# Kernel tuning notes

Measured on AMD Instinct MI355X. Metric: run time of the kernel, lower is better.

Reference implementation:

```python
import jax, jax.numpy as jnp
import numpy as np

B, T, I = 64, 512, 128
H, R, DA, C = 256, 20, 50, 10

def setup_inputs() -> dict:
    key = jax.random.key(0)
    ks = jax.random.split(key, 8)
    s = 0.05
    return {
        "x": jax.random.normal(ks[0], (B, T, I), dtype=jnp.float32),
        "W_ih": jax.random.normal(ks[1], (I, 4 * H), dtype=jnp.float32) * s,
        "W_hh": jax.random.normal(ks[2], (H, 4 * H), dtype=jnp.float32) * s,
        "b": jnp.zeros((4 * H,), dtype=jnp.float32),
        "W1": jax.random.normal(ks[3], (DA, I), dtype=jnp.float32) * s,
        "b1": jnp.zeros((DA,), dtype=jnp.float32),
        "W2": jax.random.normal(ks[4], (R, DA), dtype=jnp.float32) * s,
        "b2": jnp.zeros((R,), dtype=jnp.float32),
        "Wfc": jax.random.normal(ks[5], (C, H), dtype=jnp.float32) * s,
        "bfc": jnp.zeros((C,), dtype=jnp.float32),
    }

def reference(x, W_ih, W_hh, b, W1, b1, W2, b2, Wfc, bfc):
    # Dropout is identity (eval mode). Attention scores for all timesteps at once.
    bsz, seq, inp = x.shape
    hid = W_hh.shape[0]
    r = W2.shape[0]
    # scores: [B, T, r]
    S = jnp.tanh(jnp.einsum('bti,di->btd', x, W1) + b1)
    S = jnp.einsum('btd,rd->btr', S, W2) + b2
    # Prefix softmax over time via cumulative sums (softmax shift-invariant,
    # use global max over time per (b, r) for stability).
    E = jnp.exp(S - jnp.max(S, axis=1, keepdims=True))          # [B, T, r]
    denom = jnp.cumsum(E, axis=1)                               # [B, T, r]
    numer = jnp.cumsum(E[:, :, :, None] * x[:, :, None, :], axis=1)  # [B, T, r, I]
    M = jnp.mean(numer / denom[:, :, :, None], axis=2)          # [B, T, I]
    # Precompute input contribution to gates for all steps.
    gx = jnp.einsum('bti,ig->btg', M, W_ih) + b                 # [B, T, 4H]
    h0 = jnp.ones((bsz, hid), dtype=x.dtype)
    c0 = jnp.ones((bsz, hid), dtype=x.dtype)

    def step(carry, g_x):
        h, c = carry
        g = g_x + h @ W_hh
        i_t = jax.nn.sigmoid(g[:, :hid])
        f_t = jax.nn.sigmoid(g[:, hid:2 * hid])
        g_t = jnp.tanh(g[:, 2 * hid:3 * hid])
        o_t = jax.nn.sigmoid(g[:, 3 * hid:])
        c = f_t * c + i_t * g_t
        h = o_t * jnp.tanh(c)
        return (h, c), None

    (h_T, _), _ = jax.lax.scan(step, (h0, c0), jnp.swapaxes(gx, 0, 1))
    logits = h_T @ Wfc.T + bfc                                  # [B, C]
    return jax.nn.softmax(logits, axis=1)
```

## Files before the change

### kernel.cpp

```cpp
#include <hip/hip_runtime.h>
#include <hip/hip_fp16.h>

#define B_   64
#define T_   512
#define I_   128
#define H_   256
#define G4_  1024
#define R_   20
#define DA_  50
#define C_   10

typedef _Float16 half2_t __attribute__((ext_vector_type(2)));
typedef _Float16 half8_t __attribute__((ext_vector_type(8)));

union H8 {
  half8_t v8;
  half2_t h2[4];
};

__device__ __forceinline__ float fsigmoid(float x) {
  return __fdividef(1.0f, 1.0f + __expf(-x));
}
__device__ __forceinline__ float ftanh(float x) {
  return 1.0f - __fdividef(2.0f, __expf(2.0f * x) + 1.0f);
}

__global__ __launch_bounds__(256) void k0_pack(const float* __restrict__ Whh,
                                               half2_t* __restrict__ Wq) {
  int idx = blockIdx.x * 256 + threadIdx.x;
  int g = idx & 1023, k2 = idx >> 10;
  half2_t h;
  h.x = (_Float16)Whh[(2 * k2) * G4_ + g];
  h.y = (_Float16)Whh[(2 * k2 + 1) * G4_ + g];
  Wq[g * 128 + k2] = h;
}

__global__ __launch_bounds__(256) void k_init(unsigned long long* __restrict__ Hx) {
  int i = blockIdx.x * 256 + threadIdx.x;
  Hx[i] = 0ull;
}

__global__ __launch_bounds__(64) void k1_scores(const float* __restrict__ x,
                                                const float* __restrict__ W1,
                                                const float* __restrict__ b1,
                                                const float* __restrict__ W2,
                                                const float* __restrict__ b2,
                                                float* __restrict__ S) {
  int bt = blockIdx.x;
  int b = bt >> 9, t = bt & 511;
  int l = threadIdx.x;
  __shared__ float xs[I_];
  __shared__ float as[DA_];
  const float* xr = x + (size_t)bt * I_;
  xs[l] = xr[l];
  xs[l + 64] = xr[l + 64];
  __syncthreads();
  if (l < DA_) {
    float acc = b1[l];
    const float* wr = W1 + l * I_;
#pragma unroll 8
    for (int k = 0; k < I_; k++) acc += xs[k] * wr[k];
    as[l] = tanhf(acc);
  }
  __syncthreads();
  if (l < R_) {
    float acc = b2[l];
    const float* wr = W2 + l * DA_;
#pragma unroll 5
    for (int d = 0; d < DA_; d++) acc += as[d] * wr[d];
    S[((size_t)(b * R_ + l)) * T_ + t] = acc;
  }
}

__global__ __launch_bounds__(64) void k2_prefix(const float* __restrict__ S,
                                                float* __restrict__ E,
                                                float* __restrict__ invd) {
  int br = blockIdx.x;
  int l = threadIdx.x;
  const float* Sr = S + (size_t)br * T_;
  float v[8];
  float m = -1e30f;
#pragma unroll
  for (int c = 0; c < 8; c++) {
    v[c] = Sr[c * 64 + l];
    m = fmaxf(m, v[c]);
  }
#pragma unroll
  for (int off = 32; off; off >>= 1) m = fmaxf(m, __shfl_xor(m, off));
  float carry = 0.f;
  for (int c = 0; c < 8; c++) {
    float e = expf(v[c] - m);
    float s = e;
#pragma unroll
    for (int off = 1; off < 64; off <<= 1) {
      float u = __shfl_up(s, off);
      if (l >= off) s += u;
    }
    E[(size_t)br * T_ + c * 64 + l] = e;
    invd[(size_t)br * T_ + c * 64 + l] = 1.f / (carry + s);
    carry += __shfl(s, 63);
  }
}

__global__ __launch_bounds__(128) void k3_context(const float* __restrict__ x,
                                                  const float* __restrict__ E,
                                                  const float* __restrict__ invd,
                                                  float* __restrict__ M) {
  int b = blockIdx.x;
  int i = threadIdx.x;
  __shared__ float es[2][R_], ds[2][R_];
  float acc[R_];
#pragma unroll
  for (int r = 0; r < R_; r++) acc[r] = 0.f;
  float rE = 0.f, rD = 0.f;
  if (i < R_)
    rE = E[((size_t)(b * R_ + i)) * T_ + 0];
  else if (i < 2 * R_)
    rD = invd[((size_t)(b * R_ + (i - R_))) * T_ + 0];
  const float* xb = x + (size_t)b * T_ * I_;
  float xv = xb[i];
  int buf = 0;
  for (int t = 0; t < T_; t++) {
    if (i < R_) es[buf][i] = rE;
    else if (i < 2 * R_) ds[buf][i - R_] = rD;
    __syncthreads();
    if (t + 1 < T_) {
      if (i < R_)
        rE = E[((size_t)(b * R_ + i)) * T_ + t + 1];
      else if (i < 2 * R_)
        rD = invd[((size_t)(b * R_ + (i - R_))) * T_ + t + 1];
    }
    float xcur = xv;
    if (t + 1 < T_) xv = xb[(size_t)(t + 1) * I_ + i];
    float s = 0.f;
#pragma unroll
    for (int r = 0; r < R_; r++) {
      acc[r] += es[buf][r] * xcur;
      s += acc[r] * ds[buf][r];
    }
    M[(size_t)b * T_ * I_ + (size_t)t * I_ + i] = s * (1.0f / R_);
    buf ^= 1;
  }
}

__global__ __launch_bounds__(256) void k4_gemm(const float* __restrict__ Mm,
                                               const float* __restrict__ Wih,
                                               const float* __restrict__ bg,
                                               __half* __restrict__ gx) {
  __shared__ float As[I_][64];
  __shared__ float Bs[I_][64];
  int row0 = blockIdx.x * 64, col0 = blockIdx.y * 64;
  int tid = threadIdx.x;
#pragma unroll
  for (int ch = 0; ch < 8; ch++) {
    int fidx = ch * 256 + tid;
    int r = fidx >> 5;
    int kk = (fidx & 31) << 2;
    float4 f = ((const float4*)(Mm + (size_t)(row0 + r) * I_))[fidx & 31];
    As[kk + 0][r] = f.x;
    As[kk + 1][r] = f.y;
    As[kk + 2][r] = f.z;
    As[kk + 3][r] = f.w;
  }
#pragma unroll
  for (int ch = 0; ch < 8; ch++) {
    int fidx = ch * 256 + tid;
    int k = fidx >> 4;
    int c4 = (fidx & 15) << 2;
    float4 f = *((const float4*)(Wih + (size_t)k * G4_ + col0 + c4));
    *((float4*)&Bs[k][c4]) = f;
  }
  __syncthreads();
  int ty = tid >> 4, tx = tid & 15;
  float acc[4][4] = {};
#pragma unroll 4
  for (int k = 0; k < I_; k++) {
    float4 a = *((float4*)&As[k][ty << 2]);
    float4 bq = *((float4*)&Bs[k][tx << 2]);
    acc[0][0] += a.x * bq.x; acc[0][1] += a.x * bq.y; acc[0][2] += a.x * bq.z; acc[0][3] += a.x * bq.w;
    acc[1][0] += a.y * bq.x; acc[1][1] += a.y * bq.y; acc[1][2] += a.y * bq.z; acc[1][3] += a.y * bq.w;
    acc[2][0] += a.z * bq.x; acc[2][1] += a.z * bq.y; acc[2][2] += a.z * bq.z; acc[2][3] += a.z * bq.w;
    acc[3][0] += a.w * bq.x; acc[3][1] += a.w * bq.y; acc[3][2] += a.w * bq.z; acc[3][3] += a.w * bq.w;
  }
#pragma unroll
  for (int ii = 0; ii < 4; ii++) {
#pragma unroll
    for (int jj = 0; jj < 4; jj++) {
      int row = row0 + (ty << 2) + ii;
      int col = col0 + (tx << 2) + jj;
      gx[(size_t)row * G4_ + col] = __float2half(acc[ii][jj] + bg[col]);
    }
  }
}

__global__ __launch_bounds__(512, 2) void k5_lstm(
    const __half* __restrict__ gx, const half2_t* __restrict__ Wq,
    unsigned long long* __restrict__ Hx, float* __restrict__ hT) {
  int b = blockIdx.x & 63;
  int p = blockIdx.x >> 6;
  int tid = threadIdx.x;
  int kh = tid & 1;
  int c = tid >> 1;
  int gate = c >> 6, uloc = c & 63;
  int gcol = gate * 256 + p * 64 + uloc;

  __shared__ __align__(16) half2_t hs[H_ / 2];
  __shared__ float gsum[256];

  int qi = tid >> 5;
  int q = qi + (qi >= p ? 1 : 0);
  int d = tid & 31;

  H8 w[16];
  {
    const H8* wp = (const H8*)(Wq + (size_t)gcol * 128 + kh * 64);
#pragma unroll
    for (int i = 0; i < 16; i++) w[i].v8 = wp[i].v8;
  }
  asm volatile("" ::: "memory");

  float cstate = 1.0f;
  const __half* gxb = gx + (size_t)b * T_ * G4_;

  for (int t = 0; t < T_; t++) {
    float gxv = 0.f;
    if (!kh) gxv = (float)gxb[(size_t)t * G4_ + gcol];

    if (t == 0) {
      if (tid < 128) {
        half2_t o;
        o.x = (_Float16)1.0f;
        o.y = (_Float16)1.0f;
        hs[tid] = o;
      }
    } else if (tid < 96) {
      const unsigned long long* src =
          Hx + ((size_t)(t & 1) * 64 + b) * 128 + q * 32 + d;
      unsigned long long v;
      do {
        v = __hip_atomic_load(src, __ATOMIC_RELAXED, __HIP_MEMORY_SCOPE_AGENT);
      } while ((unsigned)(v >> 32) != (unsigned)t);
      ((unsigned*)hs)[q * 32 + d] = (unsigned)v;
    }
    __syncthreads();

    float a0 = 0.f, a1 = 0.f, a2 = 0.f, a3 = 0.f;
#pragma unroll
    for (int i = 0; i < 16; i++) {
      H8 hv;
      hv.v8 = *(const half8_t*)(hs + kh * 64 + i * 4);
      a0 = __builtin_amdgcn_fdot2(w[i].h2[0], hv.h2[0], a0, false);
      a1 = __builtin_amdgcn_fdot2(w[i].h2[1], hv.h2[1], a1, false);
      a2 = __builtin_amdgcn_fdot2(w[i].h2[2], hv.h2[2], a2, false);
      a3 = __builtin_amdgcn_fdot2(w[i].h2[3], hv.h2[3], a3, false);
    }
    float s = (a0 + a1) + (a2 + a3);
    s += __shfl_xor(s, 1);
    if (!kh) gsum[c] = s + gxv;
    __syncthreads();

    if (tid < 64) {
      float vi = gsum[tid], vf = gsum[64 + tid], vg = gsum[128 + tid],
            vo = gsum[192 + tid];
      vi = fsigmoid(vi);
      vf = fsigmoid(vf);
      vo = fsigmoid(vo);
      vg = ftanh(vg);
      cstate = vf * cstate + vi * vg;
      float h = vo * ftanh(cstate);
      unsigned hu = (unsigned)__half_as_ushort(__float2half(h));
      ((unsigned short*)hs)[p * 64 + tid] = (unsigned short)hu;
      unsigned hup = (unsigned)__shfl_xor((int)hu, 1);
      if (!(tid & 1) && (t + 1 < T_)) {
        unsigned long long pkt =
            (unsigned long long)(hu | (hup << 16)) |
            ((unsigned long long)(unsigned)(t + 1) << 32);
        unsigned long long* dst =
            Hx + ((size_t)((t + 1) & 1) * 64 + b) * 128 + p * 32 + (tid >> 1);
        __hip_atomic_store(dst, pkt, __ATOMIC_RELAXED,
                           __HIP_MEMORY_SCOPE_AGENT);
      }
      if (t == T_ - 1) hT[b * H_ + p * 64 + tid] = h;
    }
  }
}

__global__ __launch_bounds__(64) void k6_head(const float* __restrict__ hT,
                                              const float* __restrict__ Wfc,
                                              const float* __restrict__ bfc,
                                              float* __restrict__ out) {
  int b = blockIdx.x, l = threadIdx.x;
  const float* h = hT + b * H_;
  float p[C_];
#pragma unroll
  for (int c = 0; c < C_; c++) p[c] = 0.f;
#pragma unroll
  for (int q = 0; q < 4; q++) {
    float hv = h[q * 64 + l];
#pragma unroll
    for (int c = 0; c < C_; c++) p[c] += hv * Wfc[c * H_ + q * 64 + l];
  }
#pragma unroll
  for (int c = 0; c < C_; c++)
    for (int off = 32; off; off >>= 1) p[c] += __shfl_xor(p[c], off);
  if (l == 0) {
    float m = -1e30f, e[C_], sum = 0.f;
    for (int c = 0; c < C_; c++) { p[c] += bfc[c]; m = fmaxf(m, p[c]); }
    for (int c = 0; c < C_; c++) { e[c] = expf(p[c] - m); sum += e[c]; }
    for (int c = 0; c < C_; c++) out[b * C_ + c] = e[c] / sum;
  }
}

extern "C" void kernel_launch(void* const* d_in, const int* in_sizes, int n_in,
                              void* d_out, int out_size, void* d_ws, size_t ws_size,
                              hipStream_t stream) {
  const float* x   = (const float*)d_in[0];
  const float* Wih = (const float*)d_in[1];
  const float* Whh = (const float*)d_in[2];
  const float* bg  = (const float*)d_in[3];
  const float* W1  = (const float*)d_in[4];
  const float* b1  = (const float*)d_in[5];
  const float* W2  = (const float*)d_in[6];
  const float* b2  = (const float*)d_in[7];
  const float* Wfc = (const float*)d_in[8];
  const float* bfc = (const float*)d_in[9];
  float* out = (float*)d_out;

  float* wsf = (float*)d_ws;
  unsigned long long* Hx = (unsigned long long*)wsf;
  float* S    = wsf;
  float* E    = wsf + 655360;
  float* INVD = wsf + 1310720;
  float* Mm   = wsf + 1966080;
  float* hT   = wsf + 6160384;
  half2_t* Wq = (half2_t*)(wsf + 6176768);
  __half* gx  = (__half*)(wsf + 6307840);

  hipLaunchKernelGGL(k0_pack,   dim3(512),      dim3(256), 0, stream, Whh, Wq);
  hipLaunchKernelGGL(k1_scores, dim3(B_ * T_),  dim3(64),  0, stream, x, W1, b1, W2, b2, S);
  hipLaunchKernelGGL(k2_prefix, dim3(B_ * R_),  dim3(64),  0, stream, S, E, INVD);
  hipLaunchKernelGGL(k3_context,dim3(B_),       dim3(128), 0, stream, x, E, INVD, Mm);
  hipLaunchKernelGGL(k4_gemm,   dim3(512, 16),  dim3(256), 0, stream, Mm, Wih, bg, gx);
  hipLaunchKernelGGL(k_init,    dim3(64),       dim3(256), 0, stream, Hx);
  hipLaunchKernelGGL(k5_lstm,   dim3(256),      dim3(512), 0, stream, gx, Wq, Hx, hT);
  hipLaunchKernelGGL(k6_head,   dim3(B_),       dim3(64),  0, stream, hT, Wfc, bfc, out);
}
```

Measured before the change: 1.407 ms.

## Tile score GEMM, chunk context scan over time, and shuffle-based LSTM gate combine

```diff
diff --git a/kernel.cpp b/kernel.cpp
--- a/kernel.cpp
+++ b/kernel.cpp
@@ -13,11 +13,6 @@
 typedef _Float16 half2_t __attribute__((ext_vector_type(2)));
 typedef _Float16 half8_t __attribute__((ext_vector_type(8)));
 
-union H8 {
-  half8_t v8;
-  half2_t h2[4];
-};
-
 __device__ __forceinline__ float fsigmoid(float x) {
   return __fdividef(1.0f, 1.0f + __expf(-x));
 }
@@ -40,35 +35,68 @@
   Hx[i] = 0ull;
 }
 
-__global__ __launch_bounds__(64) void k1_scores(const float* __restrict__ x,
-                                                const float* __restrict__ W1,
-                                                const float* __restrict__ b1,
-                                                const float* __restrict__ W2,
-                                                const float* __restrict__ b2,
-                                                float* __restrict__ S) {
-  int bt = blockIdx.x;
+__global__ __launch_bounds__(256) void k1_scores(const float* __restrict__ x,
+                                                 const float* __restrict__ W1,
+                                                 const float* __restrict__ b1,
+                                                 const float* __restrict__ W2,
+                                                 const float* __restrict__ b2,
+                                                 float* __restrict__ S) {
+  __shared__ float xs[64][129];
+  __shared__ float w1s[128][64];
+  __shared__ float a1s[64][53];
+  int blk = blockIdx.x;
+  int tid = threadIdx.x;
+  int row0 = blk * 64;
+  const float4* xv = (const float4*)(x + (size_t)row0 * I_);
+#pragma unroll
+  for (int ch = 0; ch < 8; ch++) {
+    int fidx = ch * 256 + tid;
+    int r = fidx >> 5, k4 = (fidx & 31) << 2;
+    float4 f = xv[fidx];
+    xs[r][k4] = f.x; xs[r][k4 + 1] = f.y; xs[r][k4 + 2] = f.z; xs[r][k4 + 3] = f.w;
+  }
+  const float4* w1v = (const float4*)W1;
+#pragma unroll
+  for (int ch = 0; ch < 7; ch++) {
+    int fidx = ch * 256 + tid;
+    if (fidx < 1600) {
+      int d = fidx >> 5, k4 = (fidx & 31) << 2;
+      float4 f = w1v[fidx];
+      w1s[k4][d] = f.x; w1s[k4 + 1][d] = f.y; w1s[k4 + 2][d] = f.z; w1s[k4 + 3][d] = f.w;
+    }
+  }
+  __syncthreads();
+  int ty = tid >> 4, tx = tid & 15;
+  float acc[4][4] = {};
+#pragma unroll 4
+  for (int k = 0; k < I_; k++) {
+    float a0 = xs[4 * ty][k], a1 = xs[4 * ty + 1][k];
+    float a2 = xs[4 * ty + 2][k], a3 = xs[4 * ty + 3][k];
+    float4 bq = *(const float4*)&w1s[k][tx << 2];
+    acc[0][0] += a0 * bq.x; acc[0][1] += a0 * bq.y; acc[0][2] += a0 * bq.z; acc[0][3] += a0 * bq.w;
+    acc[1][0] += a1 * bq.x; acc[1][1] += a1 * bq.y; acc[1][2] += a1 * bq.z; acc[1][3] += a1 * bq.w;
+    acc[2][0] += a2 * bq.x; acc[2][1] += a2 * bq.y; acc[2][2] += a2 * bq.z; acc[2][3] += a2 * bq.w;
+    acc[3][0] += a3 * bq.x; acc[3][1] += a3 * bq.y; acc[3][2] += a3 * bq.z; acc[3][3] += a3 * bq.w;
+  }
+#pragma unroll
+  for (int i = 0; i < 4; i++) {
+#pragma unroll
+    for (int j = 0; j < 4; j++) {
+      int col = (tx << 2) + j;
+      if (col < DA_) a1s[4 * ty + i][col] = tanhf(acc[i][j] + b1[col]);
+    }
+  }
+  __syncthreads();
+  int row = tid & 63, rq = tid >> 6;
+  int bt = row0 + row;
   int b = bt >> 9, t = bt & 511;
-  int l = threadIdx.x;
-  __shared__ float xs[I_];
-  __shared__ float as[DA_];
-  const float* xr = x + (size_t)bt * I_;
-  xs[l] = xr[l];
-  xs[l + 64] = xr[l + 64];
-  __syncthreads();
-  if (l < DA_) {
-    float acc = b1[l];
-    const float* wr = W1 + l * I_;
-#pragma unroll 8
-    for (int k = 0; k < I_; k++) acc += xs[k] * wr[k];
-    as[l] = tanhf(acc);
-  }
-  __syncthreads();
-  if (l < R_) {
-    float acc = b2[l];
-    const float* wr = W2 + l * DA_;
-#pragma unroll 5
-    for (int d = 0; d < DA_; d++) acc += as[d] * wr[d];
-    S[((size_t)(b * R_ + l)) * T_ + t] = acc;
+#pragma unroll
+  for (int m = 0; m < 5; m++) {
+    int r = rq + (m << 2);
+    float acc2 = b2[r];
+#pragma unroll 10
+    for (int d = 0; d < DA_; d++) acc2 += a1s[row][d] * W2[r * DA_ + d];
+    S[((size_t)(b * R_ + r)) * T_ + t] = acc2;
   }
 }
 
@@ -102,43 +130,93 @@
   }
 }
 
-__global__ __launch_bounds__(128) void k3_context(const float* __restrict__ x,
-                                                  const float* __restrict__ E,
-                                                  const float* __restrict__ invd,
-                                                  float* __restrict__ M) {
-  int b = blockIdx.x;
+__global__ __launch_bounds__(128) void k3a(const float* __restrict__ x,
+                                           const float* __restrict__ E,
+                                           float* __restrict__ P) {
+  int b = blockIdx.x >> 3, c = blockIdx.x & 7;
   int i = threadIdx.x;
+  int t0 = c * 64;
+  __shared__ float es[2][R_];
+  float acc[R_];
+#pragma unroll
+  for (int r = 0; r < R_; r++) acc[r] = 0.f;
+  float rE = 0.f;
+  if (i < R_) rE = E[((size_t)(b * R_ + i)) * T_ + t0];
+  const float* xb = x + (size_t)b * T_ * I_;
+  float xv = xb[(size_t)t0 * I_ + i];
+  int buf = 0;
+  for (int tt = 0; tt < 64; tt++) {
+    if (i < R_) es[buf][i] = rE;
+    __syncthreads();
+    if (tt + 1 < 64) {
+      if (i < R_) rE = E[((size_t)(b * R_ + i)) * T_ + t0 + tt + 1];
+    }
+    float xcur = xv;
+    if (tt + 1 < 64) xv = xb[(size_t)(t0 + tt + 1) * I_ + i];
+#pragma unroll
+    for (int r = 0; r < R_; r++) acc[r] += es[buf][r] * xcur;
+    buf ^= 1;
+  }
+#pragma unroll
+  for (int r = 0; r < R_; r++)
+    P[(size_t)((b * 8 + c) * R_ + r) * I_ + i] = acc[r];
+}
+
+__global__ __launch_bounds__(256) void k3b(float* __restrict__ P) {
+  int gid = blockIdx.x * 256 + threadIdx.x;
+  int i = gid & 127;
+  int r = (gid >> 7) % R_;
+  int b = gid / (R_ * I_);
+  float s = 0.f;
+#pragma unroll
+  for (int c = 0; c < 8; c++) {
+    size_t idx = (size_t)((b * 8 + c) * R_ + r) * I_ + i;
+    float v = P[idx];
+    P[idx] = s;
+    s += v;
+  }
+}
+
+__global__ __launch_bounds__(128) void k3c(const float* __restrict__ x,
+                                           const float* __restrict__ E,
+                                           const float* __restrict__ invd,
+                                           const float* __restrict__ P,
+                                           float* __restrict__ M) {
+  int b = blockIdx.x >> 3, c = blockIdx.x & 7;
+  int i = threadIdx.x;
+  int t0 = c * 64;
   __shared__ float es[2][R_], ds[2][R_];
   float acc[R_];
 #pragma unroll
-  for (int r = 0; r < R_; r++) acc[r] = 0.f;
+  for (int r = 0; r < R_; r++)
+    acc[r] = P[(size_t)((b * 8 + c) * R_ + r) * I_ + i];
   float rE = 0.f, rD = 0.f;
   if (i < R_)
-    rE = E[((size_t)(b * R_ + i)) * T_ + 0];
+    rE = E[((size_t)(b * R_ + i)) * T_ + t0];
   else if (i < 2 * R_)
-    rD = invd[((size_t)(b * R_ + (i - R_))) * T_ + 0];
+    rD = invd[((size_t)(b * R_ + (i - R_))) * T_ + t0];
   const float* xb = x + (size_t)b * T_ * I_;
-  float xv = xb[i];
+  float xv = xb[(size_t)t0 * I_ + i];
   int buf = 0;
-  for (int t = 0; t < T_; t++) {
+  for (int tt = 0; tt < 64; tt++) {
     if (i < R_) es[buf][i] = rE;
     else if (i < 2 * R_) ds[buf][i - R_] = rD;
     __syncthreads();
-    if (t + 1 < T_) {
+    if (tt + 1 < 64) {
       if (i < R_)
-        rE = E[((size_t)(b * R_ + i)) * T_ + t + 1];
+        rE = E[((size_t)(b * R_ + i)) * T_ + t0 + tt + 1];
       else if (i < 2 * R_)
-        rD = invd[((size_t)(b * R_ + (i - R_))) * T_ + t + 1];
+        rD = invd[((size_t)(b * R_ + (i - R_))) * T_ + t0 + tt + 1];
     }
     float xcur = xv;
-    if (t + 1 < T_) xv = xb[(size_t)(t + 1) * I_ + i];
+    if (tt + 1 < 64) xv = xb[(size_t)(t0 + tt + 1) * I_ + i];
     float s = 0.f;
 #pragma unroll
     for (int r = 0; r < R_; r++) {
       acc[r] += es[buf][r] * xcur;
       s += acc[r] * ds[buf][r];
     }
-    M[(size_t)b * T_ * I_ + (size_t)t * I_ + i] = s * (1.0f / R_);
+    M[(size_t)b * T_ * I_ + (size_t)(t0 + tt) * I_ + i] = s * (1.0f / R_);
     buf ^= 1;
   }
 }
@@ -193,31 +271,40 @@
   }
 }
 
+union WREG {
+  unsigned u[64];
+  half2_t h[64];
+  uint4 q[16];
+};
+
 __global__ __launch_bounds__(512, 2) void k5_lstm(
     const __half* __restrict__ gx, const half2_t* __restrict__ Wq,
     unsigned long long* __restrict__ Hx, float* __restrict__ hT) {
   int b = blockIdx.x & 63;
   int p = blockIdx.x >> 6;
   int tid = threadIdx.x;
-  int kh = tid & 1;
-  int c = tid >> 1;
-  int gate = c >> 6, uloc = c & 63;
-  int gcol = gate * 256 + p * 64 + uloc;
-
-  __shared__ __align__(16) half2_t hs[H_ / 2];
-  __shared__ float gsum[256];
+  int wave = tid >> 6;
+  int lane = tid & 63;
+  int kh = lane & 1;
+  int gate = (lane >> 1) & 3;
+  int uw = lane >> 3;
+  int u = wave * 8 + uw;
+  int gcol = gate * H_ + p * 64 + u;
+
+  __shared__ __align__(16) unsigned hsU[2][128];
 
   int qi = tid >> 5;
-  int q = qi + (qi >= p ? 1 : 0);
-  int d = tid & 31;
-
-  H8 w[16];
+  int q_ = qi + (qi >= p ? 1 : 0);
+  int d_ = tid & 31;
+
+  WREG w;
   {
-    const H8* wp = (const H8*)(Wq + (size_t)gcol * 128 + kh * 64);
-#pragma unroll
-    for (int i = 0; i < 16; i++) w[i].v8 = wp[i].v8;
-  }
-  asm volatile("" ::: "memory");
+    const uint4* wp = (const uint4*)(Wq + (size_t)gcol * 128 + kh * 64);
+#pragma unroll
+    for (int i = 0; i < 16; i++) w.q[i] = wp[i];
+  }
+#pragma unroll
+  for (int j = 0; j < 64; j++) asm volatile("" : "+v"(w.u[j]));
 
   float cstate = 1.0f;
   const __half* gxb = gx + (size_t)b * T_ * G4_;
@@ -227,60 +314,59 @@
     if (!kh) gxv = (float)gxb[(size_t)t * G4_ + gcol];
 
     if (t == 0) {
-      if (tid < 128) {
-        half2_t o;
-        o.x = (_Float16)1.0f;
-        o.y = (_Float16)1.0f;
-        hs[tid] = o;
-      }
+      if (tid < 128) hsU[0][tid] = 0x3C003C00u;
     } else if (tid < 96) {
       const unsigned long long* src =
-          Hx + ((size_t)(t & 1) * 64 + b) * 128 + q * 32 + d;
+          Hx + ((size_t)(t & 1) * 64 + b) * 128 + q_ * 32 + d_;
       unsigned long long v;
       do {
         v = __hip_atomic_load(src, __ATOMIC_RELAXED, __HIP_MEMORY_SCOPE_AGENT);
       } while ((unsigned)(v >> 32) != (unsigned)t);
-      ((unsigned*)hs)[q * 32 + d] = (unsigned)v;
+      hsU[t & 1][q_ * 32 + d_] = (unsigned)v;
     }
     __syncthreads();
 
+    const half2_t* hb = (const half2_t*)hsU[t & 1] + kh * 64;
     float a0 = 0.f, a1 = 0.f, a2 = 0.f, a3 = 0.f;
 #pragma unroll
     for (int i = 0; i < 16; i++) {
-      H8 hv;
-      hv.v8 = *(const half8_t*)(hs + kh * 64 + i * 4);
-      a0 = __builtin_amdgcn_fdot2(w[i].h2[0], hv.h2[0], a0, false);
-      a1 = __builtin_amdgcn_fdot2(w[i].h2[1], hv.h2[1], a1, false);
-      a2 = __builtin_amdgcn_fdot2(w[i].h2[2], hv.h2[2], a2, false);
-      a3 = __builtin_amdgcn_fdot2(w[i].h2[3], hv.h2[3], a3, false);
+      half8_t hv = *(const half8_t*)(hb + i * 4);
+      half2_t h0 = ((half2_t*)&hv)[0], h1 = ((half2_t*)&hv)[1];
+      half2_t h2 = ((half2_t*)&hv)[2], h3 = ((half2_t*)&hv)[3];
+      a0 = __builtin_amdgcn_fdot2(w.h[4 * i + 0], h0, a0, false);
+      a1 = __builtin_amdgcn_fdot2(w.h[4 * i + 1], h1, a1, false);
+      a2 = __builtin_amdgcn_fdot2(w.h[4 * i + 2], h2, a2, false);
+      a3 = __builtin_amdgcn_fdot2(w.h[4 * i + 3], h3, a3, false);
     }
     float s = (a0 + a1) + (a2 + a3);
     s += __shfl_xor(s, 1);
-    if (!kh) gsum[c] = s + gxv;
-    __syncthreads();
-
-    if (tid < 64) {
-      float vi = gsum[tid], vf = gsum[64 + tid], vg = gsum[128 + tid],
-            vo = gsum[192 + tid];
-      vi = fsigmoid(vi);
-      vf = fsigmoid(vf);
-      vo = fsigmoid(vo);
-      vg = ftanh(vg);
+    s += gxv;
+
+    float f1 = __shfl_down(s, 2);
+    float f2 = __shfl_down(s, 4);
+    float f3 = __shfl_down(s, 6);
+    unsigned hu = 0;
+    if ((lane & 7) == 0) {
+      float vi = fsigmoid(s);
+      float vf = fsigmoid(f1);
+      float vg = ftanh(f2);
+      float vo = fsigmoid(f3);
       cstate = vf * cstate + vi * vg;
       float h = vo * ftanh(cstate);
-      unsigned hu = (unsigned)__half_as_ushort(__float2half(h));
-      ((unsigned short*)hs)[p * 64 + tid] = (unsigned short)hu;
-      unsigned hup = (unsigned)__shfl_xor((int)hu, 1);
-      if (!(tid & 1) && (t + 1 < T_)) {
-        unsigned long long pkt =
-            (unsigned long long)(hu | (hup << 16)) |
-            ((unsigned long long)(unsigned)(t + 1) << 32);
-        unsigned long long* dst =
-            Hx + ((size_t)((t + 1) & 1) * 64 + b) * 128 + p * 32 + (tid >> 1);
-        __hip_atomic_store(dst, pkt, __ATOMIC_RELAXED,
-                           __HIP_MEMORY_SCOPE_AGENT);
-      }
-      if (t == T_ - 1) hT[b * H_ + p * 64 + tid] = h;
+      hu = (unsigned)__half_as_ushort(__float2half(h));
+      if (t == T_ - 1) hT[b * H_ + p * 64 + u] = h;
+    }
+    unsigned hup = (unsigned)__shfl_down((int)hu, 8);
+    if ((lane & 15) == 0 && (t + 1) < T_) {
+      unsigned h2pack = hu | (hup << 16);
+      int slot = p * 32 + wave * 4 + (lane >> 4);
+      unsigned long long pkt =
+          (unsigned long long)h2pack |
+          ((unsigned long long)(unsigned)(t + 1) << 32);
+      unsigned long long* dst =
+          Hx + ((size_t)((t + 1) & 1) * 64 + b) * 128 + slot;
+      __hip_atomic_store(dst, pkt, __ATOMIC_RELAXED, __HIP_MEMORY_SCOPE_AGENT);
+      hsU[(t + 1) & 1][slot] = h2pack;
     }
   }
 }
@@ -335,13 +421,16 @@
   float* hT   = wsf + 6160384;
   half2_t* Wq = (half2_t*)(wsf + 6176768);
   __half* gx  = (__half*)(wsf + 6307840);
-
-  hipLaunchKernelGGL(k0_pack,   dim3(512),      dim3(256), 0, stream, Whh, Wq);
-  hipLaunchKernelGGL(k1_scores, dim3(B_ * T_),  dim3(64),  0, stream, x, W1, b1, W2, b2, S);
-  hipLaunchKernelGGL(k2_prefix, dim3(B_ * R_),  dim3(64),  0, stream, S, E, INVD);
-  hipLaunchKernelGGL(k3_context,dim3(B_),       dim3(128), 0, stream, x, E, INVD, Mm);
-  hipLaunchKernelGGL(k4_gemm,   dim3(512, 16),  dim3(256), 0, stream, Mm, Wih, bg, gx);
-  hipLaunchKernelGGL(k_init,    dim3(64),       dim3(256), 0, stream, Hx);
-  hipLaunchKernelGGL(k5_lstm,   dim3(256),      dim3(512), 0, stream, gx, Wq, Hx, hT);
-  hipLaunchKernelGGL(k6_head,   dim3(B_),       dim3(64),  0, stream, hT, Wfc, bfc, out);
-}
+  float* P    = wsf + 6307840;
+
+  hipLaunchKernelGGL(k0_pack,   dim3(512),     dim3(256), 0, stream, Whh, Wq);
+  hipLaunchKernelGGL(k1_scores, dim3(512),     dim3(256), 0, stream, x, W1, b1, W2, b2, S);
+  hipLaunchKernelGGL(k2_prefix, dim3(B_ * R_), dim3(64),  0, stream, S, E, INVD);
+  hipLaunchKernelGGL(k3a,       dim3(512),     dim3(128), 0, stream, x, E, P);
+  hipLaunchKernelGGL(k3b,       dim3(640),     dim3(256), 0, stream, P);
+  hipLaunchKernelGGL(k3c,       dim3(512),     dim3(128), 0, stream, x, E, INVD, P, Mm);
+  hipLaunchKernelGGL(k4_gemm,   dim3(512, 16), dim3(256), 0, stream, Mm, Wih, bg, gx);
+  hipLaunchKernelGGL(k_init,    dim3(64),      dim3(256), 0, stream, Hx);
+  hipLaunchKernelGGL(k5_lstm,   dim3(256),     dim3(512), 0, stream, gx, Wq, Hx, hT);
+  hipLaunchKernelGGL(k6_head,   dim3(B_),      dim3(64),  0, stream, hT, Wfc, bfc, out);
+}
```

After: 1.140 ms. 1.23x faster.
